# Performance work log

Measured on AMD Instinct MI355X. Metric: run time of the kernel, lower is better.

The kernel has to match this reference:

```python
import jax, jax.numpy as jnp
import numpy as np

L, WIDTH, H, B, S = 3, 4, 512, 32, 512
NHW = 2
CIN = (WIDTH + 1) * H


def _windows(padded, off0):
    # padded: [B, S+2W, H] -> [B, S, (W+1)*H], window k covers padded[:, off0+k : off0+k+S]
    return jnp.concatenate([padded[:, off0 + k: off0 + k + S] for k in range(WIDTH + 1)], axis=-1)


def _highway(x, Ws, bs):
    # Ws: [NHW, H, 2H], bs: [NHW, 2H]. AllenNLP Highway: gate*x + (1-gate)*relu(nonlin)
    for j in range(NHW):
        proj = x @ Ws[j] + bs[j]
        nonlin, gate = jnp.split(proj, 2, axis=-1)
        g = jax.nn.sigmoid(gate)
        x = g * x + (1.0 - g) * jax.nn.relu(nonlin)
    return x


def setup_inputs() -> dict:
    key = jax.random.key(0)
    ks = jax.random.split(key, 13)
    inputs = jax.random.normal(ks[0], (B, S, H), dtype=jnp.float32)
    mask = jnp.ones((B, S), dtype=jnp.int32)
    fwd_pads = jax.random.normal(ks[1], (L, WIDTH, H), dtype=jnp.float32)
    bwd_pads = jax.random.normal(ks[2], (L, WIDTH, H), dtype=jnp.float32)
    fwd_W = jax.random.normal(ks[3], (L, CIN, H), dtype=jnp.float32) * 0.02
    bwd_W = jax.random.normal(ks[4], (L, CIN, H), dtype=jnp.float32) * 0.02
    fwd_b = jnp.zeros((L, H), dtype=jnp.float32)
    bwd_b = jnp.zeros((L, H), dtype=jnp.float32)
    fwd_hw_W = jax.random.normal(ks[5], (L, NHW, H, 2 * H), dtype=jnp.float32) * 0.04
    bwd_hw_W = jax.random.normal(ks[6], (L, NHW, H, 2 * H), dtype=jnp.float32) * 0.04
    fwd_hw_b = jnp.zeros((L, NHW, 2 * H), dtype=jnp.float32)
    bwd_hw_b = jnp.zeros((L, NHW, 2 * H), dtype=jnp.float32)
    return {"inputs": inputs, "mask": mask, "fwd_pads": fwd_pads, "bwd_pads": bwd_pads,
            "fwd_W": fwd_W, "fwd_b": fwd_b, "bwd_W": bwd_W, "bwd_b": bwd_b,
            "fwd_hw_W": fwd_hw_W, "fwd_hw_b": fwd_hw_b, "bwd_hw_W": bwd_hw_W, "bwd_hw_b": bwd_hw_b}


def reference(inputs, mask, fwd_pads, bwd_pads, fwd_W, fwd_b, bwd_W, bwd_b,
              fwd_hw_W, fwd_hw_b, bwd_hw_W, bwd_hw_b):
    f_seq = inputs
    b_seq = inputs
    outs = []
    for i in range(L):
        pf = jnp.broadcast_to(fwd_pads[i], (B, WIDTH, H))
        pb = jnp.broadcast_to(bwd_pads[i], (B, WIDTH, H))
        pad_f = jnp.concatenate([pf, f_seq, pb], axis=1)  # [B, S+2W, H]
        pad_b = jnp.concatenate([pf, b_seq, pb], axis=1)
        # forward windows start at offset 0 (positions t-W..t); backward at offset W (t..t+W)
        f_in = _windows(pad_f, 0)       # [B, S, (W+1)*H]
        b_in = _windows(pad_b, WIDTH)
        f = jax.nn.relu(f_in @ fwd_W[i] + fwd_b[i])
        f = _highway(f, fwd_hw_W[i], fwd_hw_b[i])
        b = jax.nn.relu(b_in @ bwd_W[i] + bwd_b[i])
        b = _highway(b, bwd_hw_W[i], bwd_hw_b[i])
        f_seq, b_seq = f, b
        outs.append(jnp.concatenate([f, b], axis=-1))
    return jnp.stack(outs, axis=0)  # [L, B, S, 2H]
```

## Files before the change

kernel.cpp:

```cpp
#include <hip/hip_runtime.h>
#include <hip/hip_fp16.h>
#include <cstdint>
#include <cstddef>

constexpr int HD   = 512;
constexpr int SQ   = 512;
constexpr int NB   = 32;
constexpr int LAY  = 3;
constexpr int WID  = 4;
constexpr int KIN  = (WID + 1) * HD;
constexpr int PROW = SQ + 2 * WID;
constexpr int MR   = NB * SQ;
constexpr int PSTR = NB * PROW * HD;

typedef _Float16 f16x8 __attribute__((ext_vector_type(8)));
typedef float    f32x4 __attribute__((ext_vector_type(4)));

#define VMCNT(n) asm volatile("s_waitcnt vmcnt(" #n ")" ::: "memory")
#define LGKM0()  asm volatile("s_waitcnt lgkmcnt(0)" ::: "memory")
#define SBAR()   asm volatile("s_barrier" ::: "memory")

__device__ __forceinline__ void gld16(void* lds, const void* g) {
  __builtin_amdgcn_global_load_lds(
      (__attribute__((address_space(1))) void*)(g),
      (__attribute__((address_space(3))) void*)(lds),
      16, 0, 0);
}

__device__ __forceinline__ void stage_reg(_Float16* dst, const _Float16* src0,
                                          int rstride, int tid) {
#pragma unroll
  for (int j = 0; j < 2; ++j) {
    const int l = j * 512 + tid;
    const int r = l >> 2;
    const int c = ((l & 3) ^ ((r >> 1) & 3)) << 3;
    gld16(dst + (size_t)l * 8, src0 + (size_t)r * rstride + c);
  }
}

__device__ __forceinline__ f16x8 rdfrag(const _Float16* reg, int row, int q) {
  return *(const f16x8*)&reg[row * 32 + ((q ^ ((row >> 1) & 3)) << 3)];
}

__global__ void transpose_w2(const float* __restrict__ inF, const float* __restrict__ inB,
                             _Float16* __restrict__ outF, _Float16* __restrict__ outB,
                             int R, int C, int nsl, int ilv) {
  __shared__ float tile[32][33];
  const int z = blockIdx.z;
  const float* in = (z < nsl) ? inF : inB;
  _Float16* out   = (z < nsl) ? outF : outB;
  const int sl    = (z < nsl) ? z : z - nsl;
  const size_t base = (size_t)sl * R * C;
  const int r0 = blockIdx.y * 32, c0 = blockIdx.x * 32;
  const int tx = threadIdx.x, ty = threadIdx.y;
  const int half = C >> 1;
#pragma unroll
  for (int j = 0; j < 32; j += 8)
    tile[ty + j][tx] = in[base + (size_t)(r0 + ty + j) * C + (c0 + tx)];
  __syncthreads();
#pragma unroll
  for (int j = 0; j < 32; j += 8) {
    const int c = c0 + ty + j;
    const int cc = ilv ? (((c & (half - 1)) << 1) | (c >= half ? 1 : 0)) : c;
    out[base + (size_t)cc * R + (r0 + tx)] = (_Float16)tile[tx][ty + j];
  }
}

__global__ void init_interior(const float4* __restrict__ in,
                              _Float16* __restrict__ padF, _Float16* __restrict__ padB) {
  const size_t idx = (size_t)blockIdx.x * 256 + threadIdx.x;
  float4 v = in[idx];
  const size_t e = idx * 4;
  const int h = (int)(e & (HD - 1));
  const size_t bt = e >> 9;
  const int t = (int)(bt & (SQ - 1));
  const int b = (int)(bt >> 9);
  const size_t o = ((size_t)(b * PROW + WID + t)) * HD + h;
  union { _Float16 hh[4]; uint2 u; } pk;
  pk.hh[0] = (_Float16)v.x; pk.hh[1] = (_Float16)v.y;
  pk.hh[2] = (_Float16)v.z; pk.hh[3] = (_Float16)v.w;
  *(uint2*)&padF[o] = pk.u;
  *(uint2*)&padB[o] = pk.u;
}

__global__ void fill_all_pads(const float* __restrict__ fpads, const float* __restrict__ bpads,
                              _Float16* __restrict__ padF, _Float16* __restrict__ padB) {
  const int idx = blockIdx.x * 256 + threadIdx.x;
  const int h  = idx & (HD - 1);
  const int w  = (idx >> 9) & 3;
  const int b  = (idx >> 11) & 31;
  const int fb = (idx >> 16) & 1;
  const int l  = idx >> 17;
  const float v = fb ? bpads[l * WID * HD + w * HD + h] : fpads[l * WID * HD + w * HD + h];
  const int row = fb ? (SQ + WID + w) : w;
  const size_t o = (size_t)l * PSTR + ((size_t)(b * PROW + row)) * HD + h;
  const _Float16 hv = (_Float16)v;
  padF[o] = hv;
  padB[o] = hv;
}

__global__ __launch_bounds__(512, 2)
void conv_gemm(const _Float16* __restrict__ padFp, const _Float16* __restrict__ padBp,
               const _Float16* __restrict__ WtF, const _Float16* __restrict__ WtB,
               const float* __restrict__ biasF, const float* __restrict__ biasB,
               _Float16* __restrict__ tF, _Float16* __restrict__ tB) {
  constexpr int NT = KIN / 64;
  __shared__ alignas(16) _Float16 LDSA[65536];

  const int id = blockIdx.x;
  const int lg = (id & 7) * 32 + (id >> 3);
  const int dir = lg >> 7;
  const int nt  = (lg >> 6) & 1;
  const int mt  = lg & 63;

  const _Float16* pad = dir ? padBp : padFp;
  const _Float16* Wt  = dir ? WtB : WtF;
  const float* bias   = dir ? biasB : biasF;
  _Float16* outT      = dir ? tB : tF;
  const int off = dir ? WID : 0;

  const int m0 = mt * 256, n0 = nt * 256;
  const int b  = m0 >> 9, t0 = m0 & (SQ - 1);
  const int arow0 = b * PROW + t0 + off;

  const int tid  = threadIdx.x;
  const int lane = tid & 63, wv = tid >> 6;
  const int wm = wv >> 2, wn = wv & 3;
  const int lr = lane & 15, q = lane >> 4;

  f32x4 acc[8][4] = {};

  auto As = [&](int reg, int kk) {
    const int kseg = kk >> 9, h0 = kk & (HD - 1);
    stage_reg(LDSA + reg * 8192, pad + (size_t)(arow0 + kseg) * HD + h0, HD, tid);
  };
  auto Bs = [&](int reg, int kk) {
    stage_reg(LDSA + reg * 8192, Wt + (size_t)n0 * KIN + kk, KIN, tid);
  };

  As(0, 0);  Bs(1, 0);  As(2, 32); Bs(3, 32);
  As(4, 64); Bs(5, 64); As(6, 96);

#pragma unroll 2
  for (int kt = 0; kt < NT; ++kt) {
    const int bf_ = (kt & 1) * 4, of_ = 4 - bf_;
    const _Float16* A0 = LDSA + (bf_ + 0) * 8192;
    const _Float16* B0 = LDSA + (bf_ + 1) * 8192;
    const _Float16* A1 = LDSA + (bf_ + 2) * 8192;
    const _Float16* B1 = LDSA + (bf_ + 3) * 8192;
    const int k1 = (kt + 1 < NT ? kt + 1 : NT - 1) * 64;
    const int k2 = (kt + 2 < NT ? kt + 2 : NT - 1) * 64;

    f16x8 aF[8], bF[2];

    VMCNT(10);
    Bs(of_ + 3, k1 + 32);
    SBAR();
#pragma unroll
    for (int mi = 0; mi < 8; ++mi) aF[mi] = rdfrag(A0, wm * 128 + mi * 16 + lr, q);
#pragma unroll
    for (int nj = 0; nj < 2; ++nj) bF[nj] = rdfrag(B0, wn * 64 + nj * 16 + lr, q);
    __builtin_amdgcn_s_setprio(1);
#pragma unroll
    for (int mi = 0; mi < 8; ++mi)
#pragma unroll
      for (int nj = 0; nj < 2; ++nj)
        acc[mi][nj] = __builtin_amdgcn_mfma_f32_16x16x32_f16(aF[mi], bF[nj], acc[mi][nj], 0, 0, 0);
    __builtin_amdgcn_s_setprio(0);
    LGKM0();
    SBAR();

    As(bf_ + 0, k2);
    SBAR();
#pragma unroll
    for (int nj = 0; nj < 2; ++nj) bF[nj] = rdfrag(B0, wn * 64 + (nj + 2) * 16 + lr, q);
    __builtin_amdgcn_s_setprio(1);
#pragma unroll
    for (int mi = 0; mi < 8; ++mi)
#pragma unroll
      for (int nj = 0; nj < 2; ++nj)
        acc[mi][nj + 2] = __builtin_amdgcn_mfma_f32_16x16x32_f16(aF[mi], bF[nj], acc[mi][nj + 2], 0, 0, 0);
    __builtin_amdgcn_s_setprio(0);
    LGKM0();
    SBAR();

    VMCNT(10);
    Bs(bf_ + 1, k2);
    SBAR();
#pragma unroll
    for (int mi = 0; mi < 8; ++mi) aF[mi] = rdfrag(A1, wm * 128 + mi * 16 + lr, q);
#pragma unroll
    for (int nj = 0; nj < 2; ++nj) bF[nj] = rdfrag(B1, wn * 64 + nj * 16 + lr, q);
    __builtin_amdgcn_s_setprio(1);
#pragma unroll
    for (int mi = 0; mi < 8; ++mi)
#pragma unroll
      for (int nj = 0; nj < 2; ++nj)
        acc[mi][nj] = __builtin_amdgcn_mfma_f32_16x16x32_f16(aF[mi], bF[nj], acc[mi][nj], 0, 0, 0);
    __builtin_amdgcn_s_setprio(0);
    LGKM0();
    SBAR();

    As(bf_ + 2, k2 + 32);
    SBAR();
#pragma unroll
    for (int nj = 0; nj < 2; ++nj) bF[nj] = rdfrag(B1, wn * 64 + (nj + 2) * 16 + lr, q);
    __builtin_amdgcn_s_setprio(1);
#pragma unroll
    for (int mi = 0; mi < 8; ++mi)
#pragma unroll
      for (int nj = 0; nj < 2; ++nj)
        acc[mi][nj + 2] = __builtin_amdgcn_mfma_f32_16x16x32_f16(aF[mi], bF[nj], acc[mi][nj + 2], 0, 0, 0);
    __builtin_amdgcn_s_setprio(0);
    LGKM0();
    SBAR();
  }

  VMCNT(0);
  SBAR();
  _Float16* E = LDSA;
#pragma unroll
  for (int nj = 0; nj < 4; ++nj) {
    const int col = wn * 64 + nj * 16 + lr;
    const float bv = bias[n0 + col];
#pragma unroll
    for (int mi = 0; mi < 8; ++mi)
#pragma unroll
      for (int g = 0; g < 4; ++g) {
        const int row = wm * 128 + mi * 16 + q * 4 + g;
        float v = acc[mi][nj][g] + bv;
        v = v > 0.f ? v : 0.f;
        E[row * 256 + col] = (_Float16)v;
      }
  }
  LGKM0();
  SBAR();
#pragma unroll
  for (int j = 0; j < 16; ++j) {
    const int cid = j * 512 + tid;
    const int row = cid >> 5, c = cid & 31;
    f16x8 v8 = *(const f16x8*)&E[row * 256 + c * 8];
    *(f16x8*)&outT[(size_t)(m0 + row) * HD + n0 + c * 8] = v8;
  }
}

__global__ __launch_bounds__(512, 2)
void hw_gemm(const _Float16* __restrict__ xF, const _Float16* __restrict__ xB,
             const _Float16* __restrict__ WtFp, const _Float16* __restrict__ WtBp,
             const float* __restrict__ bFp, const float* __restrict__ bBp,
             _Float16* __restrict__ oFp, _Float16* __restrict__ oBp,
             float* __restrict__ out32, int mode) {
  constexpr int NT = HD / 64;
  __shared__ alignas(16) _Float16 LDSA[65536];

  const int id = blockIdx.x;
  const int lg = (id & 7) * 64 + (id >> 3);
  const int dir = lg >> 8;
  const int r2  = lg & 255;
  const int nt  = r2 >> 6, mt = r2 & 63;

  const _Float16* x  = dir ? xB : xF;
  const _Float16* Wt = dir ? WtBp : WtFp;
  const float* bias  = dir ? bBp : bFp;
  _Float16* oh       = dir ? oBp : oFp;

  const int m0 = mt * 256, n0 = nt * 256;

  const int tid  = threadIdx.x;
  const int lane = tid & 63, wv = tid >> 6;
  const int wm = wv >> 2, wn = wv & 3;
  const int lr = lane & 15, q = lane >> 4;

  f32x4 acc[8][4] = {};

  auto As = [&](int reg, int kk) {
    stage_reg(LDSA + reg * 8192, x + (size_t)m0 * HD + kk, HD, tid);
  };
  auto Bs = [&](int reg, int kk) {
    stage_reg(LDSA + reg * 8192, Wt + (size_t)n0 * HD + kk, HD, tid);
  };

  As(0, 0);  Bs(1, 0);  As(2, 32); Bs(3, 32);
  As(4, 64); Bs(5, 64); As(6, 96);

#pragma unroll 2
  for (int kt = 0; kt < NT; ++kt) {
    const int bf_ = (kt & 1) * 4, of_ = 4 - bf_;
    const _Float16* A0 = LDSA + (bf_ + 0) * 8192;
    const _Float16* B0 = LDSA + (bf_ + 1) * 8192;
    const _Float16* A1 = LDSA + (bf_ + 2) * 8192;
    const _Float16* B1 = LDSA + (bf_ + 3) * 8192;
    const int k1 = (kt + 1 < NT ? kt + 1 : NT - 1) * 64;
    const int k2 = (kt + 2 < NT ? kt + 2 : NT - 1) * 64;

    f16x8 aF[8], bF[2];

    VMCNT(10);
    Bs(of_ + 3, k1 + 32);
    SBAR();
#pragma unroll
    for (int mi = 0; mi < 8; ++mi) aF[mi] = rdfrag(A0, wm * 128 + mi * 16 + lr, q);
#pragma unroll
    for (int nj = 0; nj < 2; ++nj) bF[nj] = rdfrag(B0, wn * 64 + nj * 16 + lr, q);
    __builtin_amdgcn_s_setprio(1);
#pragma unroll
    for (int mi = 0; mi < 8; ++mi)
#pragma unroll
      for (int nj = 0; nj < 2; ++nj)
        acc[mi][nj] = __builtin_amdgcn_mfma_f32_16x16x32_f16(aF[mi], bF[nj], acc[mi][nj], 0, 0, 0);
    __builtin_amdgcn_s_setprio(0);
    LGKM0();
    SBAR();

    As(bf_ + 0, k2);
    SBAR();
#pragma unroll
    for (int nj = 0; nj < 2; ++nj) bF[nj] = rdfrag(B0, wn * 64 + (nj + 2) * 16 + lr, q);
    __builtin_amdgcn_s_setprio(1);
#pragma unroll
    for (int mi = 0; mi < 8; ++mi)
#pragma unroll
      for (int nj = 0; nj < 2; ++nj)
        acc[mi][nj + 2] = __builtin_amdgcn_mfma_f32_16x16x32_f16(aF[mi], bF[nj], acc[mi][nj + 2], 0, 0, 0);
    __builtin_amdgcn_s_setprio(0);
    LGKM0();
    SBAR();

    VMCNT(10);
    Bs(bf_ + 1, k2);
    SBAR();
#pragma unroll
    for (int mi = 0; mi < 8; ++mi) aF[mi] = rdfrag(A1, wm * 128 + mi * 16 + lr, q);
#pragma unroll
    for (int nj = 0; nj < 2; ++nj) bF[nj] = rdfrag(B1, wn * 64 + nj * 16 + lr, q);
    __builtin_amdgcn_s_setprio(1);
#pragma unroll
    for (int mi = 0; mi < 8; ++mi)
#pragma unroll
      for (int nj = 0; nj < 2; ++nj)
        acc[mi][nj] = __builtin_amdgcn_mfma_f32_16x16x32_f16(aF[mi], bF[nj], acc[mi][nj], 0, 0, 0);
    __builtin_amdgcn_s_setprio(0);
    LGKM0();
    SBAR();

    As(bf_ + 2, k2 + 32);
    SBAR();
#pragma unroll
    for (int nj = 0; nj < 2; ++nj) bF[nj] = rdfrag(B1, wn * 64 + (nj + 2) * 16 + lr, q);
    __builtin_amdgcn_s_setprio(1);
#pragma unroll
    for (int mi = 0; mi < 8; ++mi)
#pragma unroll
      for (int nj = 0; nj < 2; ++nj)
        acc[mi][nj + 2] = __builtin_amdgcn_mfma_f32_16x16x32_f16(aF[mi], bF[nj], acc[mi][nj + 2], 0, 0, 0);
    __builtin_amdgcn_s_setprio(0);
    LGKM0();
    SBAR();
  }

  VMCNT(0);
  SBAR();
  _Float16* E = LDSA;
#pragma unroll
  for (int nj = 0; nj < 4; ++nj) {
    const int col = wn * 64 + nj * 16 + lr;
    const int gcol = n0 + col;
    const float bv = bias[((gcol & 1) << 9) + (gcol >> 1)];
#pragma unroll
    for (int mi = 0; mi < 8; ++mi)
#pragma unroll
      for (int g = 0; g < 4; ++g) {
        const int row = wm * 128 + mi * 16 + q * 4 + g;
        E[row * 256 + col] = (_Float16)(acc[mi][nj][g] + bv);
      }
  }
  LGKM0();
  SBAR();
#pragma unroll
  for (int j = 0; j < 8; ++j) {
    const int cid = j * 512 + tid;
    const int row = cid >> 4, pc = cid & 15;
    f16x8 u = *(const f16x8*)&E[row * 256 + pc * 16];
    f16x8 v = *(const f16x8*)&E[row * 256 + pc * 16 + 8];
    const int xrow = m0 + row;
    const int oc0 = (n0 >> 1) + pc * 8;
    f16x8 xv8 = *(const f16x8*)&x[(size_t)xrow * HD + oc0];
    f16x8 o8;
    float of[8];
#pragma unroll
    for (int e = 0; e < 8; ++e) {
      float nl = (e < 4) ? (float)u[2 * e]     : (float)v[2 * e - 8];
      float gz = (e < 4) ? (float)u[2 * e + 1] : (float)v[2 * e - 7];
      nl = nl > 0.f ? nl : 0.f;
      const float gt = 1.f / (1.f + __expf(-gz));
      const float o = gt * (float)xv8[e] + (1.f - gt) * nl;
      of[e] = o;
      o8[e] = (_Float16)o;
    }
    if (mode == 0) {
      *(f16x8*)&oh[(size_t)xrow * HD + oc0] = o8;
    } else {
      if (mode == 1) {
        const int bb = xrow >> 9, tt = xrow & (SQ - 1);
        *(f16x8*)&oh[((size_t)(bb * PROW + WID + tt)) * HD + oc0] = o8;
      }
      float* op = out32 + (size_t)xrow * (2 * HD) + dir * HD + oc0;
      *(float4*)op = make_float4(of[0], of[1], of[2], of[3]);
      *(float4*)(op + 4) = make_float4(of[4], of[5], of[6], of[7]);
    }
  }
}

extern "C" void kernel_launch(void* const* d_in, const int* in_sizes, int n_in,
                              void* d_out, int out_size, void* d_ws, size_t ws_size,
                              hipStream_t stream) {
  const float* inputs   = (const float*)d_in[0];
  const float* fwd_pads = (const float*)d_in[2];
  const float* bwd_pads = (const float*)d_in[3];
  const float* fwd_W    = (const float*)d_in[4];
  const float* fwd_b    = (const float*)d_in[5];
  const float* bwd_W    = (const float*)d_in[6];
  const float* bwd_b    = (const float*)d_in[7];
  const float* fwd_hw_W = (const float*)d_in[8];
  const float* fwd_hw_b = (const float*)d_in[9];
  const float* bwd_hw_W = (const float*)d_in[10];
  const float* bwd_hw_b = (const float*)d_in[11];
  float* out = (float*)d_out;

  char* p = (char*)d_ws;
  auto take = [&](size_t n) { char* r = p; p += (n + 255) & ~(size_t)255; return r; };

  _Float16* padF = (_Float16*)take((size_t)LAY * PSTR * 2);
  _Float16* padB = (_Float16*)take((size_t)LAY * PSTR * 2);
  _Float16* tF   = (_Float16*)take((size_t)MR * HD * 2);
  _Float16* tB   = (_Float16*)take((size_t)MR * HD * 2);
  _Float16* uF   = (_Float16*)take((size_t)MR * HD * 2);
  _Float16* uB   = (_Float16*)take((size_t)MR * HD * 2);
  _Float16* WtcF = (_Float16*)take((size_t)LAY * HD * KIN * 2);
  _Float16* WtcB = (_Float16*)take((size_t)LAY * HD * KIN * 2);
  _Float16* WthF = (_Float16*)take((size_t)LAY * 2 * (2 * HD) * HD * 2);
  _Float16* WthB = (_Float16*)take((size_t)LAY * 2 * (2 * HD) * HD * 2);

  transpose_w2<<<dim3(HD / 32, KIN / 32, 2 * LAY), dim3(32, 8), 0, stream>>>(
      fwd_W, bwd_W, WtcF, WtcB, KIN, HD, LAY, 0);
  transpose_w2<<<dim3((2 * HD) / 32, HD / 32, 2 * LAY * 2), dim3(32, 8), 0, stream>>>(
      fwd_hw_W, bwd_hw_W, WthF, WthB, HD, 2 * HD, LAY * 2, 1);

  init_interior<<<(NB * SQ * HD / 4) / 256, 256, 0, stream>>>((const float4*)inputs, padF, padB);
  fill_all_pads<<<(LAY * 2 * NB * WID * HD) / 256, 256, 0, stream>>>(fwd_pads, bwd_pads, padF, padB);

  for (int i = 0; i < LAY; ++i) {
    _Float16* pF = padF + (size_t)i * PSTR;
    _Float16* pB = padB + (size_t)i * PSTR;
    const int nx = (i + 1 < LAY) ? (i + 1) : 0;
    _Float16* nF = padF + (size_t)nx * PSTR;
    _Float16* nB = padB + (size_t)nx * PSTR;

    conv_gemm<<<dim3(256), dim3(512), 0, stream>>>(
        pF, pB,
        WtcF + (size_t)i * HD * KIN, WtcB + (size_t)i * HD * KIN,
        fwd_b + (size_t)i * HD, bwd_b + (size_t)i * HD, tF, tB);
    hw_gemm<<<dim3(512), dim3(512), 0, stream>>>(
        tF, tB,
        WthF + (size_t)(i * 2 + 0) * (2 * HD) * HD, WthB + (size_t)(i * 2 + 0) * (2 * HD) * HD,
        fwd_hw_b + (size_t)(i * 2 + 0) * (2 * HD), bwd_hw_b + (size_t)(i * 2 + 0) * (2 * HD),
        uF, uB, nullptr, 0);
    hw_gemm<<<dim3(512), dim3(512), 0, stream>>>(
        uF, uB,
        WthF + (size_t)(i * 2 + 1) * (2 * HD) * HD, WthB + (size_t)(i * 2 + 1) * (2 * HD) * HD,
        fwd_hw_b + (size_t)(i * 2 + 1) * (2 * HD), bwd_hw_b + (size_t)(i * 2 + 1) * (2 * HD),
        nF, nB, out + (size_t)i * MR * (2 * HD), (i + 1 < LAY) ? 1 : 2);
  }
}
```

Before: 899.4 us.

## Use 1024-thread blocks with single-buffered LDS pipeline and XCD-aware tile mapping

```diff
diff --git a/kernel.cpp b/kernel.cpp
--- a/kernel.cpp
+++ b/kernel.cpp
@@ -25,17 +25,6 @@
       (__attribute__((address_space(1))) void*)(g),
       (__attribute__((address_space(3))) void*)(lds),
       16, 0, 0);
-}
-
-__device__ __forceinline__ void stage_reg(_Float16* dst, const _Float16* src0,
-                                          int rstride, int tid) {
-#pragma unroll
-  for (int j = 0; j < 2; ++j) {
-    const int l = j * 512 + tid;
-    const int r = l >> 2;
-    const int c = ((l & 3) ^ ((r >> 1) & 3)) << 3;
-    gld16(dst + (size_t)l * 8, src0 + (size_t)r * rstride + c);
-  }
 }
 
 __device__ __forceinline__ f16x8 rdfrag(const _Float16* reg, int row, int q) {
@@ -99,7 +88,7 @@
   padB[o] = hv;
 }
 
-__global__ __launch_bounds__(512, 2)
+__global__ __launch_bounds__(1024, 4)
 void conv_gemm(const _Float16* __restrict__ padFp, const _Float16* __restrict__ padBp,
                const _Float16* __restrict__ WtF, const _Float16* __restrict__ WtB,
                const float* __restrict__ biasF, const float* __restrict__ biasB,
@@ -107,11 +96,11 @@
   constexpr int NT = KIN / 64;
   __shared__ alignas(16) _Float16 LDSA[65536];
 
-  const int id = blockIdx.x;
-  const int lg = (id & 7) * 32 + (id >> 3);
-  const int dir = lg >> 7;
-  const int nt  = (lg >> 6) & 1;
-  const int mt  = lg & 63;
+  const int id  = blockIdx.x;
+  const int xcd = id & 7;
+  const int dir = xcd >> 2;
+  const int nt  = (xcd >> 1) & 1;
+  const int mt  = (xcd & 1) * 32 + (id >> 3);
 
   const _Float16* pad = dir ? padBp : padFp;
   const _Float16* Wt  = dir ? WtB : WtF;
@@ -128,123 +117,116 @@
   const int wm = wv >> 2, wn = wv & 3;
   const int lr = lane & 15, q = lane >> 4;
 
-  f32x4 acc[8][4] = {};
-
-  auto As = [&](int reg, int kk) {
-    const int kseg = kk >> 9, h0 = kk & (HD - 1);
-    stage_reg(LDSA + reg * 8192, pad + (size_t)(arow0 + kseg) * HD + h0, HD, tid);
-  };
-  auto Bs = [&](int reg, int kk) {
-    stage_reg(LDSA + reg * 8192, Wt + (size_t)n0 * KIN + kk, KIN, tid);
-  };
-
-  As(0, 0);  Bs(1, 0);  As(2, 32); Bs(3, 32);
-  As(4, 64); Bs(5, 64); As(6, 96);
-
-#pragma unroll 2
+  _Float16* A0 = LDSA;
+  _Float16* B0 = LDSA + 8192;
+  _Float16* A1 = LDSA + 16384;
+  _Float16* B1 = LDSA + 24576;
+
+  const int r   = tid >> 2;
+  const int csw = ((tid & 3) ^ ((r >> 1) & 3)) << 3;
+  const _Float16* pA = pad + (size_t)(arow0 + r) * HD + csw;
+  const _Float16* pB = Wt + (size_t)(n0 + r) * KIN + csw;
+  _Float16* dA0 = A0 + tid * 8;
+  _Float16* dB0 = B0 + tid * 8;
+  _Float16* dA1 = A1 + tid * 8;
+  _Float16* dB1 = B1 + tid * 8;
+
+  f32x4 acc[4][4] = {};
+
+  gld16(dA0, pA);
+  gld16(dB0, pB);
+  gld16(dA1, pA + 32);
+  VMCNT(1);
+  SBAR();
+
+#pragma unroll 1
   for (int kt = 0; kt < NT; ++kt) {
-    const int bf_ = (kt & 1) * 4, of_ = 4 - bf_;
-    const _Float16* A0 = LDSA + (bf_ + 0) * 8192;
-    const _Float16* B0 = LDSA + (bf_ + 1) * 8192;
-    const _Float16* A1 = LDSA + (bf_ + 2) * 8192;
-    const _Float16* B1 = LDSA + (bf_ + 3) * 8192;
-    const int k1 = (kt + 1 < NT ? kt + 1 : NT - 1) * 64;
-    const int k2 = (kt + 2 < NT ? kt + 2 : NT - 1) * 64;
-
-    f16x8 aF[8], bF[2];
-
-    VMCNT(10);
-    Bs(of_ + 3, k1 + 32);
-    SBAR();
-#pragma unroll
-    for (int mi = 0; mi < 8; ++mi) aF[mi] = rdfrag(A0, wm * 128 + mi * 16 + lr, q);
+    f16x8 aF[4], bF[2];
+#pragma unroll
+    for (int mi = 0; mi < 4; ++mi) aF[mi] = rdfrag(A0, wm * 64 + mi * 16 + lr, q);
 #pragma unroll
     for (int nj = 0; nj < 2; ++nj) bF[nj] = rdfrag(B0, wn * 64 + nj * 16 + lr, q);
-    __builtin_amdgcn_s_setprio(1);
-#pragma unroll
-    for (int mi = 0; mi < 8; ++mi)
+    gld16(dB1, pB + 32);
+    SBAR(); LGKM0();
+    __builtin_amdgcn_s_setprio(1);
+#pragma unroll
+    for (int mi = 0; mi < 4; ++mi)
 #pragma unroll
       for (int nj = 0; nj < 2; ++nj)
         acc[mi][nj] = __builtin_amdgcn_mfma_f32_16x16x32_f16(aF[mi], bF[nj], acc[mi][nj], 0, 0, 0);
     __builtin_amdgcn_s_setprio(0);
-    LGKM0();
-    SBAR();
-
-    As(bf_ + 0, k2);
     SBAR();
 #pragma unroll
     for (int nj = 0; nj < 2; ++nj) bF[nj] = rdfrag(B0, wn * 64 + (nj + 2) * 16 + lr, q);
-    __builtin_amdgcn_s_setprio(1);
-#pragma unroll
-    for (int mi = 0; mi < 8; ++mi)
+    gld16(dA0, pA + 64);
+    SBAR(); LGKM0();
+    __builtin_amdgcn_s_setprio(1);
+#pragma unroll
+    for (int mi = 0; mi < 4; ++mi)
 #pragma unroll
       for (int nj = 0; nj < 2; ++nj)
         acc[mi][nj + 2] = __builtin_amdgcn_mfma_f32_16x16x32_f16(aF[mi], bF[nj], acc[mi][nj + 2], 0, 0, 0);
     __builtin_amdgcn_s_setprio(0);
-    LGKM0();
-    SBAR();
-
-    VMCNT(10);
-    Bs(bf_ + 1, k2);
-    SBAR();
-#pragma unroll
-    for (int mi = 0; mi < 8; ++mi) aF[mi] = rdfrag(A1, wm * 128 + mi * 16 + lr, q);
+    VMCNT(1);
+    SBAR();
+#pragma unroll
+    for (int mi = 0; mi < 4; ++mi) aF[mi] = rdfrag(A1, wm * 64 + mi * 16 + lr, q);
 #pragma unroll
     for (int nj = 0; nj < 2; ++nj) bF[nj] = rdfrag(B1, wn * 64 + nj * 16 + lr, q);
-    __builtin_amdgcn_s_setprio(1);
-#pragma unroll
-    for (int mi = 0; mi < 8; ++mi)
+    gld16(dB0, pB + 64);
+    SBAR(); LGKM0();
+    __builtin_amdgcn_s_setprio(1);
+#pragma unroll
+    for (int mi = 0; mi < 4; ++mi)
 #pragma unroll
       for (int nj = 0; nj < 2; ++nj)
         acc[mi][nj] = __builtin_amdgcn_mfma_f32_16x16x32_f16(aF[mi], bF[nj], acc[mi][nj], 0, 0, 0);
     __builtin_amdgcn_s_setprio(0);
-    LGKM0();
-    SBAR();
-
-    As(bf_ + 2, k2 + 32);
     SBAR();
 #pragma unroll
     for (int nj = 0; nj < 2; ++nj) bF[nj] = rdfrag(B1, wn * 64 + (nj + 2) * 16 + lr, q);
-    __builtin_amdgcn_s_setprio(1);
-#pragma unroll
-    for (int mi = 0; mi < 8; ++mi)
+    gld16(dA1, pA + 96);
+    SBAR(); LGKM0();
+    __builtin_amdgcn_s_setprio(1);
+#pragma unroll
+    for (int mi = 0; mi < 4; ++mi)
 #pragma unroll
       for (int nj = 0; nj < 2; ++nj)
         acc[mi][nj + 2] = __builtin_amdgcn_mfma_f32_16x16x32_f16(aF[mi], bF[nj], acc[mi][nj + 2], 0, 0, 0);
     __builtin_amdgcn_s_setprio(0);
-    LGKM0();
-    SBAR();
+    VMCNT(1);
+    SBAR();
+    pA += 64; pB += 64;
   }
 
   VMCNT(0);
   SBAR();
-  _Float16* E = LDSA;
 #pragma unroll
   for (int nj = 0; nj < 4; ++nj) {
     const int col = wn * 64 + nj * 16 + lr;
     const float bv = bias[n0 + col];
 #pragma unroll
-    for (int mi = 0; mi < 8; ++mi)
+    for (int mi = 0; mi < 4; ++mi)
 #pragma unroll
       for (int g = 0; g < 4; ++g) {
-        const int row = wm * 128 + mi * 16 + q * 4 + g;
+        const int row = wm * 64 + mi * 16 + q * 4 + g;
         float v = acc[mi][nj][g] + bv;
         v = v > 0.f ? v : 0.f;
-        E[row * 256 + col] = (_Float16)v;
+        LDSA[row * 256 + (((col >> 3) ^ ((row >> 2) & 7)) << 3) + (col & 7)] = (_Float16)v;
       }
   }
   LGKM0();
   SBAR();
 #pragma unroll
-  for (int j = 0; j < 16; ++j) {
-    const int cid = j * 512 + tid;
+  for (int j = 0; j < 8; ++j) {
+    const int cid = j * 1024 + tid;
     const int row = cid >> 5, c = cid & 31;
-    f16x8 v8 = *(const f16x8*)&E[row * 256 + c * 8];
+    f16x8 v8 = *(const f16x8*)&LDSA[row * 256 + ((c ^ ((row >> 2) & 7)) << 3)];
     *(f16x8*)&outT[(size_t)(m0 + row) * HD + n0 + c * 8] = v8;
   }
 }
 
-__global__ __launch_bounds__(512, 2)
+__global__ __launch_bounds__(1024, 4)
 void hw_gemm(const _Float16* __restrict__ xF, const _Float16* __restrict__ xB,
              const _Float16* __restrict__ WtFp, const _Float16* __restrict__ WtBp,
              const float* __restrict__ bFp, const float* __restrict__ bBp,
@@ -253,11 +235,11 @@
   constexpr int NT = HD / 64;
   __shared__ alignas(16) _Float16 LDSA[65536];
 
-  const int id = blockIdx.x;
-  const int lg = (id & 7) * 64 + (id >> 3);
-  const int dir = lg >> 8;
-  const int r2  = lg & 255;
-  const int nt  = r2 >> 6, mt = r2 & 63;
+  const int id  = blockIdx.x;
+  const int xcd = id & 7;
+  const int dir = xcd >> 2;
+  const int nt  = xcd & 3;
+  const int mt  = id >> 3;
 
   const _Float16* x  = dir ? xB : xF;
   const _Float16* Wt = dir ? WtBp : WtFp;
@@ -271,117 +253,113 @@
   const int wm = wv >> 2, wn = wv & 3;
   const int lr = lane & 15, q = lane >> 4;
 
-  f32x4 acc[8][4] = {};
-
-  auto As = [&](int reg, int kk) {
-    stage_reg(LDSA + reg * 8192, x + (size_t)m0 * HD + kk, HD, tid);
-  };
-  auto Bs = [&](int reg, int kk) {
-    stage_reg(LDSA + reg * 8192, Wt + (size_t)n0 * HD + kk, HD, tid);
-  };
-
-  As(0, 0);  Bs(1, 0);  As(2, 32); Bs(3, 32);
-  As(4, 64); Bs(5, 64); As(6, 96);
-
-#pragma unroll 2
+  _Float16* A0 = LDSA;
+  _Float16* B0 = LDSA + 8192;
+  _Float16* A1 = LDSA + 16384;
+  _Float16* B1 = LDSA + 24576;
+
+  const int r   = tid >> 2;
+  const int csw = ((tid & 3) ^ ((r >> 1) & 3)) << 3;
+  const _Float16* pA = x + (size_t)(m0 + r) * HD + csw;
+  const _Float16* pB = Wt + (size_t)(n0 + r) * HD + csw;
+  _Float16* dA0 = A0 + tid * 8;
+  _Float16* dB0 = B0 + tid * 8;
+  _Float16* dA1 = A1 + tid * 8;
+  _Float16* dB1 = B1 + tid * 8;
+
+  f32x4 acc[4][4] = {};
+
+  gld16(dA0, pA);
+  gld16(dB0, pB);
+  gld16(dA1, pA + 32);
+  VMCNT(1);
+  SBAR();
+
+#pragma unroll 1
   for (int kt = 0; kt < NT; ++kt) {
-    const int bf_ = (kt & 1) * 4, of_ = 4 - bf_;
-    const _Float16* A0 = LDSA + (bf_ + 0) * 8192;
-    const _Float16* B0 = LDSA + (bf_ + 1) * 8192;
-    const _Float16* A1 = LDSA + (bf_ + 2) * 8192;
-    const _Float16* B1 = LDSA + (bf_ + 3) * 8192;
-    const int k1 = (kt + 1 < NT ? kt + 1 : NT - 1) * 64;
-    const int k2 = (kt + 2 < NT ? kt + 2 : NT - 1) * 64;
-
-    f16x8 aF[8], bF[2];
-
-    VMCNT(10);
-    Bs(of_ + 3, k1 + 32);
-    SBAR();
-#pragma unroll
-    for (int mi = 0; mi < 8; ++mi) aF[mi] = rdfrag(A0, wm * 128 + mi * 16 + lr, q);
+    f16x8 aF[4], bF[2];
+#pragma unroll
+    for (int mi = 0; mi < 4; ++mi) aF[mi] = rdfrag(A0, wm * 64 + mi * 16 + lr, q);
 #pragma unroll
     for (int nj = 0; nj < 2; ++nj) bF[nj] = rdfrag(B0, wn * 64 + nj * 16 + lr, q);
-    __builtin_amdgcn_s_setprio(1);
-#pragma unroll
-    for (int mi = 0; mi < 8; ++mi)
+    gld16(dB1, pB + 32);
+    SBAR(); LGKM0();
+    __builtin_amdgcn_s_setprio(1);
+#pragma unroll
+    for (int mi = 0; mi < 4; ++mi)
 #pragma unroll
       for (int nj = 0; nj < 2; ++nj)
         acc[mi][nj] = __builtin_amdgcn_mfma_f32_16x16x32_f16(aF[mi], bF[nj], acc[mi][nj], 0, 0, 0);
     __builtin_amdgcn_s_setprio(0);
-    LGKM0();
-    SBAR();
-
-    As(bf_ + 0, k2);
     SBAR();
 #pragma unroll
     for (int nj = 0; nj < 2; ++nj) bF[nj] = rdfrag(B0, wn * 64 + (nj + 2) * 16 + lr, q);
-    __builtin_amdgcn_s_setprio(1);
-#pragma unroll
-    for (int mi = 0; mi < 8; ++mi)
+    gld16(dA0, pA + 64);
+    SBAR(); LGKM0();
+    __builtin_amdgcn_s_setprio(1);
+#pragma unroll
+    for (int mi = 0; mi < 4; ++mi)
 #pragma unroll
       for (int nj = 0; nj < 2; ++nj)
         acc[mi][nj + 2] = __builtin_amdgcn_mfma_f32_16x16x32_f16(aF[mi], bF[nj], acc[mi][nj + 2], 0, 0, 0);
     __builtin_amdgcn_s_setprio(0);
-    LGKM0();
-    SBAR();
-
-    VMCNT(10);
-    Bs(bf_ + 1, k2);
-    SBAR();
-#pragma unroll
-    for (int mi = 0; mi < 8; ++mi) aF[mi] = rdfrag(A1, wm * 128 + mi * 16 + lr, q);
+    VMCNT(1);
+    SBAR();
+#pragma unroll
+    for (int mi = 0; mi < 4; ++mi) aF[mi] = rdfrag(A1, wm * 64 + mi * 16 + lr, q);
 #pragma unroll
     for (int nj = 0; nj < 2; ++nj) bF[nj] = rdfrag(B1, wn * 64 + nj * 16 + lr, q);
-    __builtin_amdgcn_s_setprio(1);
-#pragma unroll
-    for (int mi = 0; mi < 8; ++mi)
+    gld16(dB0, pB + 64);
+    SBAR(); LGKM0();
+    __builtin_amdgcn_s_setprio(1);
+#pragma unroll
+    for (int mi = 0; mi < 4; ++mi)
 #pragma unroll
       for (int nj = 0; nj < 2; ++nj)
         acc[mi][nj] = __builtin_amdgcn_mfma_f32_16x16x32_f16(aF[mi], bF[nj], acc[mi][nj], 0, 0, 0);
     __builtin_amdgcn_s_setprio(0);
-    LGKM0();
-    SBAR();
-
-    As(bf_ + 2, k2 + 32);
     SBAR();
 #pragma unroll
     for (int nj = 0; nj < 2; ++nj) bF[nj] = rdfrag(B1, wn * 64 + (nj + 2) * 16 + lr, q);
-    __builtin_amdgcn_s_setprio(1);
-#pragma unroll
-    for (int mi = 0; mi < 8; ++mi)
+    gld16(dA1, pA + 96);
+    SBAR(); LGKM0();
+    __builtin_amdgcn_s_setprio(1);
+#pragma unroll
+    for (int mi = 0; mi < 4; ++mi)
 #pragma unroll
       for (int nj = 0; nj < 2; ++nj)
         acc[mi][nj + 2] = __builtin_amdgcn_mfma_f32_16x16x32_f16(aF[mi], bF[nj], acc[mi][nj + 2], 0, 0, 0);
     __builtin_amdgcn_s_setprio(0);
-    LGKM0();
-    SBAR();
+    VMCNT(1);
+    SBAR();
+    pA += 64; pB += 64;
   }
 
   VMCNT(0);
   SBAR();
-  _Float16* E = LDSA;
 #pragma unroll
   for (int nj = 0; nj < 4; ++nj) {
     const int col = wn * 64 + nj * 16 + lr;
     const int gcol = n0 + col;
     const float bv = bias[((gcol & 1) << 9) + (gcol >> 1)];
 #pragma unroll
-    for (int mi = 0; mi < 8; ++mi)
+    for (int mi = 0; mi < 4; ++mi)
 #pragma unroll
       for (int g = 0; g < 4; ++g) {
-        const int row = wm * 128 + mi * 16 + q * 4 + g;
-        E[row * 256 + col] = (_Float16)(acc[mi][nj][g] + bv);
+        const int row = wm * 64 + mi * 16 + q * 4 + g;
+        LDSA[row * 256 + (((col >> 3) ^ ((row >> 2) & 7)) << 3) + (col & 7)] =
+            (_Float16)(acc[mi][nj][g] + bv);
       }
   }
   LGKM0();
   SBAR();
 #pragma unroll
-  for (int j = 0; j < 8; ++j) {
-    const int cid = j * 512 + tid;
+  for (int j = 0; j < 4; ++j) {
+    const int cid = j * 1024 + tid;
     const int row = cid >> 4, pc = cid & 15;
-    f16x8 u = *(const f16x8*)&E[row * 256 + pc * 16];
-    f16x8 v = *(const f16x8*)&E[row * 256 + pc * 16 + 8];
+    const int s = (row >> 2) & 7;
+    f16x8 u = *(const f16x8*)&LDSA[row * 256 + (((pc * 2) ^ s) << 3)];
+    f16x8 v = *(const f16x8*)&LDSA[row * 256 + (((pc * 2 + 1) ^ s) << 3)];
     const int xrow = m0 + row;
     const int oc0 = (n0 >> 1) + pc * 8;
     f16x8 xv8 = *(const f16x8*)&x[(size_t)xrow * HD + oc0];
@@ -456,16 +434,16 @@
     _Float16* nF = padF + (size_t)nx * PSTR;
     _Float16* nB = padB + (size_t)nx * PSTR;
 
-    conv_gemm<<<dim3(256), dim3(512), 0, stream>>>(
+    conv_gemm<<<dim3(256), dim3(1024), 0, stream>>>(
         pF, pB,
         WtcF + (size_t)i * HD * KIN, WtcB + (size_t)i * HD * KIN,
         fwd_b + (size_t)i * HD, bwd_b + (size_t)i * HD, tF, tB);
-    hw_gemm<<<dim3(512), dim3(512), 0, stream>>>(
+    hw_gemm<<<dim3(512), dim3(1024), 0, stream>>>(
         tF, tB,
         WthF + (size_t)(i * 2 + 0) * (2 * HD) * HD, WthB + (size_t)(i * 2 + 0) * (2 * HD) * HD,
         fwd_hw_b + (size_t)(i * 2 + 0) * (2 * HD), bwd_hw_b + (size_t)(i * 2 + 0) * (2 * HD),
         uF, uB, nullptr, 0);
-    hw_gemm<<<dim3(512), dim3(512), 0, stream>>>(
+    hw_gemm<<<dim3(512), dim3(1024), 0, stream>>>(
         uF, uB,
         WthF + (size_t)(i * 2 + 1) * (2 * HD) * HD, WthB + (size_t)(i * 2 + 1) * (2 * HD) * HD,
         fwd_hw_b + (size_t)(i * 2 + 1) * (2 * HD), bwd_hw_b + (size_t)(i * 2 + 1) * (2 * HD),
```

Measured after the change: 900.2 us. Within noise of the previous version (+0.1%).
